# Performance work log

Measured on AMD Instinct MI355X. Metric: run time of the kernel, lower is better.

Reference implementation:

```python
import jax, jax.numpy as jnp
import numpy as np

S = 4096   # decoder sequence length
T = 4096   # encoder sequence length
D = 2048   # x_size == qk_size (required for q @ k^T to typecheck)


def setup_inputs() -> dict:
    key = jax.random.key(0)
    k1, k2, k3, k4 = jax.random.split(key, 4)
    x_vectors = jax.random.normal(k1, (S, D), dtype=jnp.float32)
    enc_output = jax.random.normal(k2, (2, T, S), dtype=jnp.float32) * 0.02
    Wq = jax.random.normal(k3, (D, D), dtype=jnp.float32) * 0.02
    bq = jax.random.normal(k4, (D,), dtype=jnp.float32) * 0.02
    return {"x_vectors": x_vectors, "enc_output": enc_output, "Wq": Wq, "bq": bq}


def reference(x_vectors, enc_output, Wq, bq):
    # q = Linear(x): [S, D]
    q = x_vectors @ Wq.T + bq
    # k, v produced by matmul of encoder-output matrices with x: [T, D]
    k = enc_output[0] @ x_vectors
    v = enc_output[1] @ x_vectors
    # attention scores [S, T], scaled by sqrt(qk_size)
    e = (q @ k.T) / jnp.sqrt(jnp.float32(D))
    # softmax over dim=1 (last axis of the rank-2 score matrix)
    a = jax.nn.softmax(e, axis=1)
    # z = a @ v^T: [S, D]
    z = a @ v
    return z
```

## Files before the change

kernel.cpp:

```cpp
#include <hip/hip_runtime.h>


typedef __attribute__((ext_vector_type(8))) __bf16 bf16x8;
typedef __attribute__((ext_vector_type(4))) float f32x4;
typedef __attribute__((ext_vector_type(8))) unsigned short ushort8v;

#define S_DIM 4096
#define T_DIM 4096
#define D_DIM 2048

__device__ __forceinline__ unsigned short f2bf(float f) {
    unsigned int u = __float_as_uint(f);
    u += 0x7fffu + ((u >> 16) & 1u);
    return (unsigned short)(u >> 16);
}

__device__ __forceinline__ void block_sync() {
    __builtin_amdgcn_sched_barrier(0);
    __builtin_amdgcn_s_barrier();
    __builtin_amdgcn_sched_barrier(0);
}

#define GL(gptr, sptr)                                                        \
    __builtin_amdgcn_global_load_lds(                                         \
        (__attribute__((address_space(1))) void*)(void*)(gptr),               \
        (__attribute__((address_space(3))) void*)(sptr), 16, 0, 0)

__device__ __forceinline__ f32x4 MFMA16(bf16x8 a, bf16x8 b, f32x4 c) {
    return __builtin_amdgcn_mfma_f32_16x16x32_bf16(a, b, c, 0, 0, 0);
}

__global__ __launch_bounds__(256)
void k_convert(const float* __restrict__ in, unsigned short* __restrict__ out, long n) {
    long i = ((long)blockIdx.x * blockDim.x + threadIdx.x) * 8;
    const long stride = (long)gridDim.x * blockDim.x * 8;
    for (; i < n; i += stride) {
        float4 a = *(const float4*)(in + i);
        float4 b = *(const float4*)(in + i + 4);
        ushort8v o;
        o[0] = f2bf(a.x); o[1] = f2bf(a.y); o[2] = f2bf(a.z); o[3] = f2bf(a.w);
        o[4] = f2bf(b.x); o[5] = f2bf(b.y); o[6] = f2bf(b.z); o[7] = f2bf(b.w);
        *(ushort8v*)(out + i) = o;
    }
}

__global__ __launch_bounds__(256)
void k_transpose_dual(const float* __restrict__ in,
                      unsigned short* __restrict__ outT,
                      unsigned short* __restrict__ outN, int R, int C) {
    __shared__ float tile[32][33];
    const int bx = blockIdx.x * 32;
    const int by = blockIdx.y * 32;
    const int tx = threadIdx.x;
    const int ty = threadIdx.y;
    #pragma unroll
    for (int i = 0; i < 32; i += 8) {
        float v = in[(long)(by + ty + i) * C + bx + tx];
        tile[ty + i][tx] = v;
        outN[(long)(by + ty + i) * C + bx + tx] = f2bf(v);
    }
    __syncthreads();
    #pragma unroll
    for (int i = 0; i < 32; i += 8)
        outT[(long)(bx + ty + i) * R + by + tx] = f2bf(tile[tx][ty + i]);
}

__global__ __launch_bounds__(256)
void k_transpose_bf(const unsigned short* __restrict__ in,
                    unsigned short* __restrict__ out, int R, int C) {
    __shared__ unsigned short tile[32][33];
    const int bx = blockIdx.x * 32;
    const int by = blockIdx.y * 32;
    const int tx = threadIdx.x;
    const int ty = threadIdx.y;
    #pragma unroll
    for (int i = 0; i < 32; i += 8)
        tile[ty + i][tx] = in[(long)(by + ty + i) * C + bx + tx];
    __syncthreads();
    #pragma unroll
    for (int i = 0; i < 32; i += 8)
        out[(long)(bx + ty + i) * R + by + tx] = tile[tx][ty + i];
}

template<bool STG, bool PF, int VMW>
__device__ __forceinline__ void seg4(
    const unsigned short* (&gA)[2], const int (&ldA)[2],
    const unsigned short* (&gB)[2], const int (&ldB)[2],
    const char* cur, const char* nxt, char* stg, int arB, int brB,
    bf16x8 (&Ac)[4], bf16x8 (&B01c)[2], bf16x8 (&B23)[2],
    bf16x8 (&An)[4], bf16x8 (&B01n)[2],
    f32x4 (&acc)[4][4])
{
    B23[0] = *(const bf16x8*)(cur + brB + 2048);
    B23[1] = *(const bf16x8*)(cur + brB + 3072);
    if constexpr (STG) {
        GL(gA[0], stg + ldA[0]); gA[0] += 32;
        GL(gA[1], stg + ldA[1]); gA[1] += 32;
    }
    block_sync();
    asm volatile("s_waitcnt lgkmcnt(2)" ::: "memory");
    __builtin_amdgcn_sched_barrier(0);
    __builtin_amdgcn_s_setprio(1);
    #pragma unroll
    for (int m = 0; m < 4; ++m) {
        acc[m][0] = MFMA16(Ac[m], B01c[0], acc[m][0]);
        acc[m][1] = MFMA16(Ac[m], B01c[1], acc[m][1]);
    }
    __builtin_amdgcn_s_setprio(0);
    if constexpr (PF) {
        #pragma unroll
        for (int m = 0; m < 4; ++m)
            An[m] = *(const bf16x8*)(nxt + arB + m * 1024);
        B01n[0] = *(const bf16x8*)(nxt + brB);
        B01n[1] = *(const bf16x8*)(nxt + brB + 1024);
    }
    if constexpr (STG) {
        GL(gB[0], stg + ldB[0]); gB[0] += 32;
        GL(gB[1], stg + ldB[1]); gB[1] += 32;
    }
    if constexpr (VMW == 4)      asm volatile("s_waitcnt vmcnt(4)" ::: "memory");
    else if constexpr (VMW == 0) asm volatile("s_waitcnt vmcnt(0)" ::: "memory");
    block_sync();
    if constexpr (PF) asm volatile("s_waitcnt lgkmcnt(6)" ::: "memory");
    else              asm volatile("s_waitcnt lgkmcnt(0)" ::: "memory");
    __builtin_amdgcn_sched_barrier(0);
    __builtin_amdgcn_s_setprio(1);
    #pragma unroll
    for (int m = 0; m < 4; ++m) {
        acc[m][2] = MFMA16(Ac[m], B23[0], acc[m][2]);
        acc[m][3] = MFMA16(Ac[m], B23[1], acc[m][3]);
    }
    __builtin_amdgcn_s_setprio(0);
}

template<int OUT_BF16, int HAS_BIAS>
__global__ __launch_bounds__(256, 2)
void k_gemm(const unsigned short* __restrict__ A,
            const unsigned short* __restrict__ B,
            const float* __restrict__ bias,
            void* __restrict__ C,
            int M, int N, int K, float alpha) {
    constexpr int LDSA = 128 * 64;
    constexpr int SLOT = LDSA + 8192;
    extern __shared__ __align__(16) char smem[];

    const int tid = threadIdx.x;
    const int l = tid & 63;
    const int w = tid >> 6;
    const int wr = w >> 1;
    const int wc = w & 1;

    const int gx = gridDim.x, gy = gridDim.y;
    const int flat = blockIdx.y * gx + blockIdx.x;
    const int per = (gx * gy) >> 3;
    const int wid = (flat & 7) * per + (flat >> 3);
    const int sc = wid / (gy * 4);
    const int rm = wid - sc * gy * 4;
    const int by = rm >> 2;
    const int bx = sc * 4 + (rm & 3);

    const long brow = (long)by * 128;
    const long bcol = (long)bx * 128;
    const int NT = K >> 5;

    const unsigned short* gA[2];
    int ldA[2];
    #pragma unroll
    for (int j = 0; j < 2; ++j) {
        const int q = (w * 2 + j) * 64 + l;
        const int R = q >> 2;
        const int c = (q & 3) ^ ((R >> 1) & 3);
        gA[j] = A + (brow + R) * (long)K + c * 8;
        ldA[j] = q * 16;
    }
    const unsigned short* gB[2];
    int ldB[2];
    #pragma unroll
    for (int j = 0; j < 2; ++j) {
        const int q = (w * 2 + j) * 64 + l;
        const int R = q >> 2;
        const int c = (q & 3) ^ ((R >> 1) & 3);
        gB[j] = B + (bcol + R) * (long)K + c * 8;
        ldB[j] = LDSA + q * 16;
    }

    const int sAB = (((l >> 4) ^ ((l >> 1) & 3)) << 4);
    const int arB = (wr * 64 + (l & 15)) * 64 + sAB;
    const int brB = LDSA + (wc * 64 + (l & 15)) * 64 + sAB;

    char* const b0 = smem;
    char* const b1 = smem + SLOT;
    char* const b2 = smem + 2 * SLOT;
    char* const b3 = smem + 3 * SLOT;

    {
        char* d = smem;
        #pragma unroll
        for (int tt = 0; tt < 3; ++tt) {
            #pragma unroll
            for (int j = 0; j < 2; ++j) { GL(gA[j], d + ldA[j]); gA[j] += 32; }
            #pragma unroll
            for (int j = 0; j < 2; ++j) { GL(gB[j], d + ldB[j]); gB[j] += 32; }
            d += SLOT;
        }
        asm volatile("s_waitcnt vmcnt(4)" ::: "memory");
        block_sync();
    }

    bf16x8 Aa[4], Ab[4], Ba[2], Bb[2], B23[2];
    #pragma unroll
    for (int m = 0; m < 4; ++m) Aa[m] = *(const bf16x8*)(b0 + arB + m * 1024);
    Ba[0] = *(const bf16x8*)(b0 + brB);
    Ba[1] = *(const bf16x8*)(b0 + brB + 1024);

    f32x4 acc[4][4] = {};
    for (int t = 0; t + 8 <= NT; t += 4) {
        seg4<true, true, 4>(gA, ldA, gB, ldB, b0, b1, b3, arB, brB,
                            Aa, Ba, B23, Ab, Bb, acc);
        seg4<true, true, 4>(gA, ldA, gB, ldB, b1, b2, b0, arB, brB,
                            Ab, Bb, B23, Aa, Ba, acc);
        seg4<true, true, 4>(gA, ldA, gB, ldB, b2, b3, b1, arB, brB,
                            Aa, Ba, B23, Ab, Bb, acc);
        seg4<true, true, 4>(gA, ldA, gB, ldB, b3, b0, b2, arB, brB,
                            Ab, Bb, B23, Aa, Ba, acc);
    }
    seg4<true,  true,  4>(gA, ldA, gB, ldB, b0, b1, b3, arB, brB,
                          Aa, Ba, B23, Ab, Bb, acc);
    seg4<false, true,  0>(gA, ldA, gB, ldB, b1, b2, b3, arB, brB,
                          Ab, Bb, B23, Aa, Ba, acc);
    seg4<false, true, -1>(gA, ldA, gB, ldB, b2, b3, b3, arB, brB,
                          Aa, Ba, B23, Ab, Bb, acc);
    seg4<false, false, -1>(gA, ldA, gB, ldB, b3, b0, b3, arB, brB,
                           Ab, Bb, B23, Aa, Ba, acc);

    const long crow0 = brow + wr * 64 + (l >> 4) * 4;
    const long ccol0 = bcol + wc * 64 + (l & 15);
    #pragma unroll
    for (int n = 0; n < 4; ++n) {
        const long col = ccol0 + n * 16;
        const float bb = HAS_BIAS ? bias[col] : 0.0f;
        #pragma unroll
        for (int m = 0; m < 4; ++m) {
            #pragma unroll
            for (int r = 0; r < 4; ++r) {
                const long row = crow0 + m * 16 + r;
                const float v = acc[m][n][r] * alpha + bb;
                if (OUT_BF16)
                    ((unsigned short*)C)[row * N + col] = f2bf(v);
                else
                    ((float*)C)[row * N + col] = v;
            }
        }
    }
}

__global__ __launch_bounds__(256)
void k_softmax_bf(const unsigned short* __restrict__ E,
                  unsigned short* __restrict__ A, int T) {
    const long row = blockIdx.x;
    const unsigned short* er = E + row * (long)T;
    const int t = threadIdx.x;
    const int l = t & 63;
    const int w = t >> 6;

    float v[16];
    float m = -3.4e38f;
    #pragma unroll
    for (int j = 0; j < 2; ++j) {
        ushort8v u = *(const ushort8v*)(er + j * 2048 + t * 8);
        #pragma unroll
        for (int i = 0; i < 8; ++i) {
            v[j * 8 + i] = __uint_as_float((unsigned int)u[i] << 16);
            m = fmaxf(m, v[j * 8 + i]);
        }
    }
    #pragma unroll
    for (int o = 32; o > 0; o >>= 1) m = fmaxf(m, __shfl_xor(m, o));

    __shared__ float redm[4];
    __shared__ float reds[4];
    if (l == 0) redm[w] = m;
    __syncthreads();
    m = fmaxf(fmaxf(redm[0], redm[1]), fmaxf(redm[2], redm[3]));

    float s = 0.f;
    #pragma unroll
    for (int i = 0; i < 16; ++i) {
        v[i] = __expf(v[i] - m);
        s += v[i];
    }
    #pragma unroll
    for (int o = 32; o > 0; o >>= 1) s += __shfl_xor(s, o);
    if (l == 0) reds[w] = s;
    __syncthreads();
    s = reds[0] + reds[1] + reds[2] + reds[3];
    const float inv = 1.0f / s;

    unsigned short* ar = A + row * (long)T;
    #pragma unroll
    for (int j = 0; j < 2; ++j) {
        ushort8v o8;
        #pragma unroll
        for (int i = 0; i < 8; ++i) o8[i] = f2bf(v[j * 8 + i] * inv);
        *(ushort8v*)(ar + j * 2048 + t * 8) = o8;
    }
}

extern "C" void kernel_launch(void* const* d_in, const int* in_sizes, int n_in,
                              void* d_out, int out_size, void* d_ws, size_t ws_size,
                              hipStream_t stream) {
    const float* x   = (const float*)d_in[0];
    const float* enc = (const float*)d_in[1];
    const float* Wq  = (const float*)d_in[2];
    const float* bq  = (const float*)d_in[3];
    float* out = (float*)d_out;
    char* ws = (char*)d_ws;

    unsigned short* abf   = (unsigned short*)(ws);
    unsigned short* xT    = (unsigned short*)(ws);
    unsigned short* xbf   = (unsigned short*)(ws + (16L << 20));
    unsigned short* wqbf  = (unsigned short*)(ws + (32L << 20));
    unsigned short* qbf   = (unsigned short*)(ws + (40L << 20));
    unsigned short* kv    = (unsigned short*)(ws + (56L << 20));
    unsigned short* vT    = (unsigned short*)(ws + (88L << 20));
    unsigned short* encbf = (unsigned short*)(ws + (104L << 20));
    unsigned short* ebf   = (unsigned short*)(ws + (104L << 20));

    k_convert<<<4096, 256, 0, stream>>>(Wq,  wqbf,  (long)D_DIM * D_DIM);
    k_convert<<<4096, 256, 0, stream>>>(enc, encbf, 2L * T_DIM * S_DIM);
    k_transpose_dual<<<dim3(D_DIM / 32, S_DIM / 32), dim3(32, 8), 0, stream>>>(
        x, xT, xbf, S_DIM, D_DIM);

    #define LAUNCH_G(OB, HB, Ap, Bp, biasp, Cp, M_, N_, K_, al)                            \
        do {                                                                               \
            constexpr int smemB = 4 * (128 * 64 + 8192);                                   \
            hipFuncSetAttribute((const void*)k_gemm<OB, HB>,                               \
                                hipFuncAttributeMaxDynamicSharedMemorySize, smemB);        \
            k_gemm<OB, HB><<<dim3((N_) / 128, (M_) / 128), 256, smemB, stream>>>(          \
                Ap, Bp, biasp, Cp, M_, N_, K_, al);                                        \
        } while (0)

    LAUNCH_G(1, 1, xbf, wqbf, bq, qbf, S_DIM, D_DIM, D_DIM, 1.0f);
    LAUNCH_G(1, 0, encbf, xT, nullptr, kv, 2 * T_DIM, D_DIM, S_DIM, 1.0f);
    k_transpose_bf<<<dim3(D_DIM / 32, T_DIM / 32), dim3(32, 8), 0, stream>>>(
        kv + (long)T_DIM * D_DIM, vT, T_DIM, D_DIM);
    LAUNCH_G(1, 0, qbf, kv, nullptr, ebf, S_DIM, T_DIM, D_DIM, 0.022097086912079608f);
    k_softmax_bf<<<S_DIM, 256, 0, stream>>>(ebf, abf, T_DIM);
    LAUNCH_G(0, 0, abf, vT, nullptr, out, S_DIM, D_DIM, T_DIM, 1.0f);
}
```

Measured before the change: 418.0 us.

## Add 256x256 8-wave GEMM kernel and widen existing GEMM to 128x256 tiles

Adds a new k_gemm8 kernel with 256x256 output tiles, 512 threads, 64-wide K steps, double-buffered LDS (128 KB) and a four-phase MFMA/load interleave. It is used for the K/V projection and QK^T GEMMs. The existing k_gemm is widened to 128x256 tiles with 8 waves and used for the Q projection and final AV GEMM. Larger tiles raise arithmetic intensity and cut global/LDS traffic per FLOP. The cost is more registers and LDS per block, which lowers occupancy, and fewer blocks for the smaller GEMMs, which risks tail effects.

```diff
diff --git a/kernel.cpp b/kernel.cpp
--- a/kernel.cpp
+++ b/kernel.cpp
@@ -29,6 +29,8 @@
 __device__ __forceinline__ f32x4 MFMA16(bf16x8 a, bf16x8 b, f32x4 c) {
     return __builtin_amdgcn_mfma_f32_16x16x32_bf16(a, b, c, 0, 0, 0);
 }
+
+#define LD8(p) (*(const bf16x8*)(p))
 
 __global__ __launch_bounds__(256)
 void k_convert(const float* __restrict__ in, unsigned short* __restrict__ out, long n) {
@@ -82,73 +84,119 @@
         out[(long)(bx + ty + i) * R + by + tx] = tile[tx][ty + i];
 }
 
-template<bool STG, bool PF, int VMW>
-__device__ __forceinline__ void seg4(
-    const unsigned short* (&gA)[2], const int (&ldA)[2],
-    const unsigned short* (&gB)[2], const int (&ldB)[2],
-    const char* cur, const char* nxt, char* stg, int arB, int brB,
-    bf16x8 (&Ac)[4], bf16x8 (&B01c)[2], bf16x8 (&B23)[2],
-    bf16x8 (&An)[4], bf16x8 (&B01n)[2],
-    f32x4 (&acc)[4][4])
+template<bool SP1, bool SP234, int V2, int V3, bool RD>
+__device__ __forceinline__ void tile64(
+    const unsigned short* __restrict__ pA, const unsigned short* __restrict__ pB,
+    long K, char* cur, char* nxt, int tid, long k1, long k2,
+    int arB0, int brB0,
+    bf16x8 (&A0)[8], bf16x8 (&A1)[8], bf16x8 (&B0)[4], bf16x8 (&B1)[4],
+    f32x4 (&acc)[8][4])
 {
-    B23[0] = *(const bf16x8*)(cur + brB + 2048);
-    B23[1] = *(const bf16x8*)(cur + brB + 3072);
-    if constexpr (STG) {
-        GL(gA[0], stg + ldA[0]); gA[0] += 32;
-        GL(gA[1], stg + ldA[1]); gA[1] += 32;
-    }
-    block_sync();
-    asm volatile("s_waitcnt lgkmcnt(2)" ::: "memory");
+    const int arB1 = arB0 ^ 64;
+    const int brB1 = brB0 ^ 64;
+    B1[0] = LD8(cur + brB0 + 4096);
+    B1[1] = LD8(cur + brB1 + 4096);
+    B1[2] = LD8(cur + brB0 + 6144);
+    B1[3] = LD8(cur + brB1 + 6144);
+    if constexpr (SP1) {
+        GL(pB + 128 * K + k1, nxt + 49152 + tid * 16);
+        GL(pB + 192 * K + k1, nxt + 57344 + tid * 16);
+    }
+    block_sync();
+    asm volatile("s_waitcnt lgkmcnt(4)" ::: "memory");
     __builtin_amdgcn_sched_barrier(0);
     __builtin_amdgcn_s_setprio(1);
     #pragma unroll
-    for (int m = 0; m < 4; ++m) {
-        acc[m][0] = MFMA16(Ac[m], B01c[0], acc[m][0]);
-        acc[m][1] = MFMA16(Ac[m], B01c[1], acc[m][1]);
-    }
+    for (int ks = 0; ks < 2; ++ks)
+        #pragma unroll
+        for (int mi = 0; mi < 4; ++mi)
+            #pragma unroll
+            for (int ni = 0; ni < 2; ++ni)
+                acc[mi][ni] = MFMA16(A0[mi * 2 + ks], B0[ni * 2 + ks], acc[mi][ni]);
     __builtin_amdgcn_s_setprio(0);
-    if constexpr (PF) {
-        #pragma unroll
-        for (int m = 0; m < 4; ++m)
-            An[m] = *(const bf16x8*)(nxt + arB + m * 1024);
-        B01n[0] = *(const bf16x8*)(nxt + brB);
-        B01n[1] = *(const bf16x8*)(nxt + brB + 1024);
-    }
-    if constexpr (STG) {
-        GL(gB[0], stg + ldB[0]); gB[0] += 32;
-        GL(gB[1], stg + ldB[1]); gB[1] += 32;
-    }
-    if constexpr (VMW == 4)      asm volatile("s_waitcnt vmcnt(4)" ::: "memory");
-    else if constexpr (VMW == 0) asm volatile("s_waitcnt vmcnt(0)" ::: "memory");
-    block_sync();
-    if constexpr (PF) asm volatile("s_waitcnt lgkmcnt(6)" ::: "memory");
+    #pragma unroll
+    for (int mi = 0; mi < 4; ++mi) {
+        A1[mi * 2 + 0] = LD8(cur + arB0 + (4 + mi) * 2048);
+        A1[mi * 2 + 1] = LD8(cur + arB1 + (4 + mi) * 2048);
+    }
+    if constexpr (SP234) {
+        GL(pB + k2, cur + 32768 + tid * 16);
+        GL(pB + 64 * K + k2, cur + 40960 + tid * 16);
+    }
+    if constexpr (V2 == 4)      asm volatile("s_waitcnt vmcnt(4)" ::: "memory");
+    else if constexpr (V2 == 2) asm volatile("s_waitcnt vmcnt(2)" ::: "memory");
+    block_sync();
+    asm volatile("s_waitcnt lgkmcnt(8)" ::: "memory");
+    __builtin_amdgcn_sched_barrier(0);
+    __builtin_amdgcn_s_setprio(1);
+    #pragma unroll
+    for (int ks = 0; ks < 2; ++ks)
+        #pragma unroll
+        for (int mi = 0; mi < 4; ++mi)
+            #pragma unroll
+            for (int ni = 0; ni < 2; ++ni)
+                acc[mi][2 + ni] = MFMA16(A0[mi * 2 + ks], B1[ni * 2 + ks], acc[mi][2 + ni]);
+    __builtin_amdgcn_s_setprio(0);
+    if constexpr (RD) {
+        #pragma unroll
+        for (int mi = 0; mi < 4; ++mi) {
+            A0[mi * 2 + 0] = LD8(nxt + arB0 + mi * 2048);
+            A0[mi * 2 + 1] = LD8(nxt + arB1 + mi * 2048);
+        }
+    }
+    if constexpr (SP234) {
+        GL(pA + k2, cur + tid * 16);
+        GL(pA + 64 * K + k2, cur + 8192 + tid * 16);
+    }
+    if constexpr (V3 == 4)      asm volatile("s_waitcnt vmcnt(4)" ::: "memory");
+    else if constexpr (V3 == 0) asm volatile("s_waitcnt vmcnt(0)" ::: "memory");
+    block_sync();
+    if constexpr (RD) asm volatile("s_waitcnt lgkmcnt(8)" ::: "memory");
     else              asm volatile("s_waitcnt lgkmcnt(0)" ::: "memory");
     __builtin_amdgcn_sched_barrier(0);
     __builtin_amdgcn_s_setprio(1);
     #pragma unroll
-    for (int m = 0; m < 4; ++m) {
-        acc[m][2] = MFMA16(Ac[m], B23[0], acc[m][2]);
-        acc[m][3] = MFMA16(Ac[m], B23[1], acc[m][3]);
-    }
+    for (int ks = 0; ks < 2; ++ks)
+        #pragma unroll
+        for (int mi = 0; mi < 4; ++mi)
+            #pragma unroll
+            for (int ni = 0; ni < 2; ++ni)
+                acc[4 + mi][ni] = MFMA16(A1[mi * 2 + ks], B0[ni * 2 + ks], acc[4 + mi][ni]);
     __builtin_amdgcn_s_setprio(0);
-}
-
-template<int OUT_BF16, int HAS_BIAS>
-__global__ __launch_bounds__(256, 2)
-void k_gemm(const unsigned short* __restrict__ A,
-            const unsigned short* __restrict__ B,
-            const float* __restrict__ bias,
-            void* __restrict__ C,
-            int M, int N, int K, float alpha) {
-    constexpr int LDSA = 128 * 64;
-    constexpr int SLOT = LDSA + 8192;
+    if constexpr (RD) {
+        B0[0] = LD8(nxt + brB0);
+        B0[1] = LD8(nxt + brB1);
+        B0[2] = LD8(nxt + brB0 + 2048);
+        B0[3] = LD8(nxt + brB1 + 2048);
+    }
+    if constexpr (SP234) {
+        GL(pA + 128 * K + k2, cur + 16384 + tid * 16);
+        GL(pA + 192 * K + k2, cur + 24576 + tid * 16);
+    }
+    block_sync();
+    __builtin_amdgcn_s_setprio(1);
+    #pragma unroll
+    for (int ks = 0; ks < 2; ++ks)
+        #pragma unroll
+        for (int mi = 0; mi < 4; ++mi)
+            #pragma unroll
+            for (int ni = 0; ni < 2; ++ni)
+                acc[4 + mi][2 + ni] = MFMA16(A1[mi * 2 + ks], B1[ni * 2 + ks], acc[4 + mi][2 + ni]);
+    __builtin_amdgcn_s_setprio(0);
+}
+
+template<int OUT_BF16>
+__global__ __launch_bounds__(512, 2)
+void k_gemm8(const unsigned short* __restrict__ A,
+             const unsigned short* __restrict__ B,
+             void* __restrict__ C,
+             int M, int N, int K, float alpha) {
     extern __shared__ __align__(16) char smem[];
-
     const int tid = threadIdx.x;
     const int l = tid & 63;
     const int w = tid >> 6;
-    const int wr = w >> 1;
-    const int wc = w & 1;
+    const int wr = w >> 2;
+    const int wc = w & 3;
 
     const int gx = gridDim.x, gy = gridDim.y;
     const int flat = blockIdx.y * gx + blockIdx.x;
@@ -159,19 +207,175 @@
     const int by = rm >> 2;
     const int bx = sc * 4 + (rm & 3);
 
+    const long brow = (long)by * 256;
+    const long bcol = (long)bx * 256;
+    const int NT = K >> 6;
+    const long Kl = K;
+
+    const int R0 = tid >> 3;
+    const int C0 = (tid & 7) ^ (R0 & 7);
+    const unsigned short* pA = A + (brow + R0) * Kl + C0 * 8;
+    const unsigned short* pB = B + (bcol + R0) * Kl + C0 * 8;
+
+    const int slot0 = (((l >> 4) ^ (l & 7)) << 4);
+    const int arB0 = (wr * 128 + (l & 15)) * 128 + slot0;
+    const int brB0 = 32768 + (wc * 64 + (l & 15)) * 128 + slot0;
+
+    char* s0 = smem;
+    char* s1 = smem + 65536;
+
+    bf16x8 A0[8], A1[8], B0[4], B1[4];
+    f32x4 acc[8][4] = {};
+
+    GL(pB,                 s0 + 32768 + tid * 16);
+    GL(pB + 64 * Kl,       s0 + 40960 + tid * 16);
+    GL(pB + 128 * Kl,      s0 + 49152 + tid * 16);
+    GL(pB + 192 * Kl,      s0 + 57344 + tid * 16);
+    GL(pA,                 s0 + tid * 16);
+    GL(pA + 64 * Kl,       s0 + 8192 + tid * 16);
+    GL(pA + 128 * Kl,      s0 + 16384 + tid * 16);
+    GL(pA + 192 * Kl,      s0 + 24576 + tid * 16);
+    GL(pB + 64,            s1 + 32768 + tid * 16);
+    GL(pB + 64 * Kl + 64,  s1 + 40960 + tid * 16);
+    GL(pA + 64,            s1 + tid * 16);
+    GL(pA + 64 * Kl + 64,  s1 + 8192 + tid * 16);
+    GL(pA + 128 * Kl + 64, s1 + 16384 + tid * 16);
+    GL(pA + 192 * Kl + 64, s1 + 24576 + tid * 16);
+    asm volatile("s_waitcnt vmcnt(6)" ::: "memory");
+    block_sync();
+    #pragma unroll
+    for (int mi = 0; mi < 4; ++mi) {
+        A0[mi * 2 + 0] = LD8(s0 + arB0 + mi * 2048);
+        A0[mi * 2 + 1] = LD8(s0 + (arB0 ^ 64) + mi * 2048);
+    }
+    B0[0] = LD8(s0 + brB0);
+    B0[1] = LD8(s0 + (brB0 ^ 64));
+    B0[2] = LD8(s0 + brB0 + 2048);
+    B0[3] = LD8(s0 + (brB0 ^ 64) + 2048);
+
+    char* cur = s0;
+    char* nxt = s1;
+    for (int t = 0; t < NT - 2; ++t) {
+        tile64<true, true, 4, 4, true>(pA, pB, Kl, cur, nxt, tid,
+                                       (long)(t + 1) << 6, (long)(t + 2) << 6,
+                                       arB0, brB0, A0, A1, B0, B1, acc);
+        char* tp = cur; cur = nxt; nxt = tp;
+    }
+    tile64<true, false, 2, 0, true>(pA, pB, Kl, cur, nxt, tid,
+                                    (long)(NT - 1) << 6, 0,
+                                    arB0, brB0, A0, A1, B0, B1, acc);
+    { char* tp = cur; cur = nxt; nxt = tp; }
+    tile64<false, false, -1, -1, false>(pA, pB, Kl, cur, nxt, tid, 0, 0,
+                                        arB0, brB0, A0, A1, B0, B1, acc);
+
+    const long crow0 = brow + wr * 128 + (l >> 4) * 4;
+    const long ccol0 = bcol + wc * 64 + (l & 15);
+    #pragma unroll
+    for (int n = 0; n < 4; ++n) {
+        const long col = ccol0 + n * 16;
+        #pragma unroll
+        for (int m = 0; m < 8; ++m) {
+            #pragma unroll
+            for (int r = 0; r < 4; ++r) {
+                const long row = crow0 + m * 16 + r;
+                const float v = acc[m][n][r] * alpha;
+                if (OUT_BF16)
+                    ((unsigned short*)C)[row * N + col] = f2bf(v);
+                else
+                    ((float*)C)[row * N + col] = v;
+            }
+        }
+    }
+}
+
+template<bool STG, bool PF, int VMW>
+__device__ __forceinline__ void seg4(
+    const unsigned short* (&gA)[1], const int (&ldA)[1],
+    const unsigned short* (&gB)[2], const int (&ldB)[2],
+    const char* cur, const char* nxt, char* stg, int arB, int brB,
+    bf16x8 (&Ac)[4], bf16x8 (&B01c)[2], bf16x8 (&B23)[2],
+    bf16x8 (&An)[4], bf16x8 (&B01n)[2],
+    f32x4 (&acc)[4][4])
+{
+    B23[0] = LD8(cur + brB + 2048);
+    B23[1] = LD8(cur + brB + 3072);
+    if constexpr (STG) {
+        GL(gA[0], stg + ldA[0]); gA[0] += 32;
+    }
+    block_sync();
+    asm volatile("s_waitcnt lgkmcnt(2)" ::: "memory");
+    __builtin_amdgcn_sched_barrier(0);
+    __builtin_amdgcn_s_setprio(1);
+    #pragma unroll
+    for (int m = 0; m < 4; ++m) {
+        acc[m][0] = MFMA16(Ac[m], B01c[0], acc[m][0]);
+        acc[m][1] = MFMA16(Ac[m], B01c[1], acc[m][1]);
+    }
+    __builtin_amdgcn_s_setprio(0);
+    if constexpr (PF) {
+        #pragma unroll
+        for (int m = 0; m < 4; ++m)
+            An[m] = LD8(nxt + arB + m * 1024);
+        B01n[0] = LD8(nxt + brB);
+        B01n[1] = LD8(nxt + brB + 1024);
+    }
+    if constexpr (STG) {
+        GL(gB[0], stg + ldB[0]); gB[0] += 32;
+        GL(gB[1], stg + ldB[1]); gB[1] += 32;
+    }
+    if constexpr (VMW == 3)      asm volatile("s_waitcnt vmcnt(3)" ::: "memory");
+    else if constexpr (VMW == 0) asm volatile("s_waitcnt vmcnt(0)" ::: "memory");
+    block_sync();
+    if constexpr (PF) asm volatile("s_waitcnt lgkmcnt(6)" ::: "memory");
+    else              asm volatile("s_waitcnt lgkmcnt(0)" ::: "memory");
+    __builtin_amdgcn_sched_barrier(0);
+    __builtin_amdgcn_s_setprio(1);
+    #pragma unroll
+    for (int m = 0; m < 4; ++m) {
+        acc[m][2] = MFMA16(Ac[m], B23[0], acc[m][2]);
+        acc[m][3] = MFMA16(Ac[m], B23[1], acc[m][3]);
+    }
+    __builtin_amdgcn_s_setprio(0);
+}
+
+template<int OUT_BF16, int HAS_BIAS>
+__global__ __launch_bounds__(512, 2)
+void k_gemm(const unsigned short* __restrict__ A,
+            const unsigned short* __restrict__ B,
+            const float* __restrict__ bias,
+            void* __restrict__ C,
+            int M, int N, int K, float alpha) {
+    constexpr int LDSA = 128 * 64;
+    constexpr int SLOT = LDSA + 16384;
+    extern __shared__ __align__(16) char smem[];
+
+    const int tid = threadIdx.x;
+    const int l = tid & 63;
+    const int w = tid >> 6;
+    const int wr = w >> 2;
+    const int wc = w & 3;
+
+    const int gx = gridDim.x, gy = gridDim.y;
+    const int flat = blockIdx.y * gx + blockIdx.x;
+    const int per = (gx * gy) >> 3;
+    const int wid = (flat & 7) * per + (flat >> 3);
+    const int sc = wid / (gy * 4);
+    const int rm = wid - sc * gy * 4;
+    const int by = rm >> 2;
+    const int bx = sc * 4 + (rm & 3);
+
     const long brow = (long)by * 128;
-    const long bcol = (long)bx * 128;
+    const long bcol = (long)bx * 256;
     const int NT = K >> 5;
 
-    const unsigned short* gA[2];
-    int ldA[2];
-    #pragma unroll
-    for (int j = 0; j < 2; ++j) {
-        const int q = (w * 2 + j) * 64 + l;
+    const unsigned short* gA[1];
+    int ldA[1];
+    {
+        const int q = w * 64 + l;
         const int R = q >> 2;
         const int c = (q & 3) ^ ((R >> 1) & 3);
-        gA[j] = A + (brow + R) * (long)K + c * 8;
-        ldA[j] = q * 16;
+        gA[0] = A + (brow + R) * (long)K + c * 8;
+        ldA[0] = q * 16;
     }
     const unsigned short* gB[2];
     int ldB[2];
@@ -197,34 +401,33 @@
         char* d = smem;
         #pragma unroll
         for (int tt = 0; tt < 3; ++tt) {
-            #pragma unroll
-            for (int j = 0; j < 2; ++j) { GL(gA[j], d + ldA[j]); gA[j] += 32; }
+            GL(gA[0], d + ldA[0]); gA[0] += 32;
             #pragma unroll
             for (int j = 0; j < 2; ++j) { GL(gB[j], d + ldB[j]); gB[j] += 32; }
             d += SLOT;
         }
-        asm volatile("s_waitcnt vmcnt(4)" ::: "memory");
+        asm volatile("s_waitcnt vmcnt(3)" ::: "memory");
         block_sync();
     }
 
     bf16x8 Aa[4], Ab[4], Ba[2], Bb[2], B23[2];
     #pragma unroll
-    for (int m = 0; m < 4; ++m) Aa[m] = *(const bf16x8*)(b0 + arB + m * 1024);
-    Ba[0] = *(const bf16x8*)(b0 + brB);
-    Ba[1] = *(const bf16x8*)(b0 + brB + 1024);
+    for (int m = 0; m < 4; ++m) Aa[m] = LD8(b0 + arB + m * 1024);
+    Ba[0] = LD8(b0 + brB);
+    Ba[1] = LD8(b0 + brB + 1024);
 
     f32x4 acc[4][4] = {};
     for (int t = 0; t + 8 <= NT; t += 4) {
-        seg4<true, true, 4>(gA, ldA, gB, ldB, b0, b1, b3, arB, brB,
+        seg4<true, true, 3>(gA, ldA, gB, ldB, b0, b1, b3, arB, brB,
                             Aa, Ba, B23, Ab, Bb, acc);
-        seg4<true, true, 4>(gA, ldA, gB, ldB, b1, b2, b0, arB, brB,
+        seg4<true, true, 3>(gA, ldA, gB, ldB, b1, b2, b0, arB, brB,
                             Ab, Bb, B23, Aa, Ba, acc);
-        seg4<true, true, 4>(gA, ldA, gB, ldB, b2, b3, b1, arB, brB,
+        seg4<true, true, 3>(gA, ldA, gB, ldB, b2, b3, b1, arB, brB,
                             Aa, Ba, B23, Ab, Bb, acc);
-        seg4<true, true, 4>(gA, ldA, gB, ldB, b3, b0, b2, arB, brB,
+        seg4<true, true, 3>(gA, ldA, gB, ldB, b3, b0, b2, arB, brB,
                             Ab, Bb, B23, Aa, Ba, acc);
     }
-    seg4<true,  true,  4>(gA, ldA, gB, ldB, b0, b1, b3, arB, brB,
+    seg4<true,  true,  3>(gA, ldA, gB, ldB, b0, b1, b3, arB, brB,
                           Aa, Ba, B23, Ab, Bb, acc);
     seg4<false, true,  0>(gA, ldA, gB, ldB, b1, b2, b3, arB, brB,
                           Ab, Bb, B23, Aa, Ba, acc);
@@ -331,20 +534,28 @@
     k_transpose_dual<<<dim3(D_DIM / 32, S_DIM / 32), dim3(32, 8), 0, stream>>>(
         x, xT, xbf, S_DIM, D_DIM);
 
-    #define LAUNCH_G(OB, HB, Ap, Bp, biasp, Cp, M_, N_, K_, al)                            \
+    #define LAUNCH_G4(OB, HB, Ap, Bp, biasp, Cp, M_, N_, K_, al)                           \
         do {                                                                               \
-            constexpr int smemB = 4 * (128 * 64 + 8192);                                   \
+            constexpr int smemB = (128 * 64 + 16384) * 4;                                  \
             hipFuncSetAttribute((const void*)k_gemm<OB, HB>,                               \
                                 hipFuncAttributeMaxDynamicSharedMemorySize, smemB);        \
-            k_gemm<OB, HB><<<dim3((N_) / 128, (M_) / 128), 256, smemB, stream>>>(          \
+            k_gemm<OB, HB><<<dim3((N_) / 256, (M_) / 128), 512, smemB, stream>>>(          \
                 Ap, Bp, biasp, Cp, M_, N_, K_, al);                                        \
         } while (0)
 
-    LAUNCH_G(1, 1, xbf, wqbf, bq, qbf, S_DIM, D_DIM, D_DIM, 1.0f);
-    LAUNCH_G(1, 0, encbf, xT, nullptr, kv, 2 * T_DIM, D_DIM, S_DIM, 1.0f);
+    #define LAUNCH_G8(OB, Ap, Bp, Cp, M_, N_, K_, al)                                      \
+        do {                                                                               \
+            hipFuncSetAttribute((const void*)k_gemm8<OB>,                                  \
+                                hipFuncAttributeMaxDynamicSharedMemorySize, 131072);       \
+            k_gemm8<OB><<<dim3((N_) / 256, (M_) / 256), 512, 131072, stream>>>(            \
+                Ap, Bp, Cp, M_, N_, K_, al);                                               \
+        } while (0)
+
+    LAUNCH_G4(1, 1, xbf, wqbf, bq, qbf, S_DIM, D_DIM, D_DIM, 1.0f);
+    LAUNCH_G8(1, encbf, xT, kv, 2 * T_DIM, D_DIM, S_DIM, 1.0f);
     k_transpose_bf<<<dim3(D_DIM / 32, T_DIM / 32), dim3(32, 8), 0, stream>>>(
         kv + (long)T_DIM * D_DIM, vT, T_DIM, D_DIM);
-    LAUNCH_G(1, 0, qbf, kv, nullptr, ebf, S_DIM, T_DIM, D_DIM, 0.022097086912079608f);
+    LAUNCH_G8(1, qbf, kv, ebf, S_DIM, T_DIM, D_DIM, 0.022097086912079608f);
     k_softmax_bf<<<S_DIM, 256, 0, stream>>>(ebf, abf, T_DIM);
-    LAUNCH_G(0, 0, abf, vT, nullptr, out, S_DIM, D_DIM, T_DIM, 1.0f);
-}
+    LAUNCH_G4(0, 0, abf, vT, nullptr, out, S_DIM, D_DIM, T_DIM, 1.0f);
+}
```

Measured after the change: 351.8 us (median of 2 runs). 1.19x faster.
